# Kernel optimization log

Hardware: AMD Instinct MI355X
Metric: run time of the kernel (lower is better)

Reference implementation:

```python
import jax, jax.numpy as jnp
import numpy as np
from jax import lax

N, IN_C, H, W = 8, 256, 100, 100
MID_C = 256
RATIOS = (0.5, 1.0, 2.0)
SCALES = (8, 16, 32)
FEAT_STRIDE = 16
BASE_SIZE = 16.0
K = len(RATIOS) * len(SCALES)
NMS_THRESH = 0.7
PRE_NMS = 3000
POST_NMS = 300
MIN_SIZE = 16.0


def _anchor_base():
    py = px = BASE_SIZE / 2.0
    ab = np.zeros((K, 4), np.float32)
    i = 0
    for r in RATIOS:
        for s in SCALES:
            h = BASE_SIZE * s * np.sqrt(r)
            w = BASE_SIZE * s * np.sqrt(1.0 / r)
            ab[i] = [py - h / 2.0, px - w / 2.0, py + h / 2.0, px + w / 2.0]
            i += 1
    return ab


def _all_anchors():
    ab = _anchor_base()
    sy = np.arange(H, dtype=np.float32) * FEAT_STRIDE
    sx = np.arange(W, dtype=np.float32) * FEAT_STRIDE
    yy, xx = np.meshgrid(sy, sx, indexing="ij")
    shifts = np.stack([yy.ravel(), xx.ravel(), yy.ravel(), xx.ravel()], 1)  # [HW,4]
    anchors = (shifts[:, None, :] + ab[None, :, :]).reshape(-1, 4)  # (h,w,k) order -> [K*H*W,4]
    return jnp.asarray(anchors)


def _conv(x, w, b, pad):
    y = lax.conv_general_dilated(x, w, (1, 1), [(pad, pad), (pad, pad)],
                                 dimension_numbers=("NCHW", "OIHW", "NCHW"))
    return y + b[None, :, None, None]


def _decode(anchors, loc):  # reg2bbox: boxes in [y1,x1,y2,x2], loc = [dy,dx,dh,dw]
    ah = anchors[:, 2] - anchors[:, 0]
    aw = anchors[:, 3] - anchors[:, 1]
    ay = anchors[:, 0] + 0.5 * ah
    ax = anchors[:, 1] + 0.5 * aw
    dy, dx, dh, dw = loc[:, 0], loc[:, 1], loc[:, 2], loc[:, 3]
    cy = dy * ah + ay
    cx = dx * aw + ax
    h = jnp.exp(dh) * ah
    w = jnp.exp(dw) * aw
    return jnp.stack([cy - 0.5 * h, cx - 0.5 * w, cy + 0.5 * h, cx + 0.5 * w], 1)


def _greedy_nms(boxes, valid):  # boxes sorted by score desc; returns keep mask
    P = boxes.shape[0]
    y1, x1, y2, x2 = boxes[:, 0], boxes[:, 1], boxes[:, 2], boxes[:, 3]
    areas = (y2 - y1) * (x2 - x1)
    idx = jnp.arange(P)

    def body(i, keep):
        yy1 = jnp.maximum(y1[i], y1)
        xx1 = jnp.maximum(x1[i], x1)
        yy2 = jnp.minimum(y2[i], y2)
        xx2 = jnp.minimum(x2[i], x2)
        inter = jnp.maximum(yy2 - yy1, 0.0) * jnp.maximum(xx2 - xx1, 0.0)
        iou = inter / (areas[i] + areas - inter + 1e-9)
        suppress = (iou > NMS_THRESH) & (idx > i) & keep[i]
        return keep & (~suppress)

    return lax.fori_loop(0, P, body, valid)


def _propose(anchors, scores, loc, img_w, img_h):
    boxes = _decode(anchors, loc)
    y1 = jnp.clip(boxes[:, 0], 0.0, img_h)
    y2 = jnp.clip(boxes[:, 2], 0.0, img_h)
    x1 = jnp.clip(boxes[:, 1], 0.0, img_w)
    x2 = jnp.clip(boxes[:, 3], 0.0, img_w)
    boxes = jnp.stack([y1, x1, y2, x2], 1)
    big = ((y2 - y1) >= MIN_SIZE) & ((x2 - x1) >= MIN_SIZE)
    s = jnp.where(big, scores, -1.0)  # push filtered boxes to the bottom (softmax scores in [0,1])
    order = jnp.argsort(-s)[:PRE_NMS]
    b = boxes[order]
    v = big[order]
    keep = _greedy_nms(lax.stop_gradient(b), v)
    # kept boxes first, preserving score order (matches torchvision nms index order)
    rank = jnp.where(keep, jnp.arange(PRE_NMS), PRE_NMS + jnp.arange(PRE_NMS))
    sel = jnp.argsort(rank)[:POST_NMS]
    roi = b[sel] * keep[sel][:, None].astype(b.dtype)  # zero-pad suppressed slots
    return roi


def reference(x, w1, b1, wc, bc, wr, br, img_width, img_height):
    h = jax.nn.relu(_conv(x, w1, b1, 1))
    cls = _conv(h, wc, bc, 0)  # [N,2K,H,W]
    cls = jnp.transpose(cls, (0, 2, 3, 1)).reshape(N, -1, 2)  # [N,KHW,2]
    fg = jax.nn.softmax(cls, axis=-1)[:, :, 1]  # [N,KHW]
    cls_out = jnp.transpose(cls, (0, 2, 1))  # [N,2,KHW]
    reg = _conv(h, wr, br, 0)
    reg = jnp.transpose(reg, (0, 2, 3, 1)).reshape(N, -1, 4)  # [N,KHW,4]
    anchors = _all_anchors()
    rois = jax.vmap(_propose, in_axes=(None, 0, 0, None, None))(
        anchors, fg, reg, float(img_width), float(img_height))  # [N,POST_NMS,4]
    roi_inds = jnp.repeat(jnp.arange(N, dtype=jnp.float32), POST_NMS)
    return cls_out, reg, rois.reshape(-1, 4), roi_inds, anchors


def setup_inputs() -> dict:
    key = jax.random.key(0)
    ks = jax.random.split(key, 4)
    std = 0.01
    return {
        "x": jax.random.normal(ks[0], (N, IN_C, H, W), jnp.float32),
        "w1": std * jax.random.normal(ks[1], (MID_C, IN_C, 3, 3), jnp.float32),
        "b1": jnp.zeros((MID_C,), jnp.float32),
        "wc": std * jax.random.normal(ks[2], (2 * K, MID_C, 1, 1), jnp.float32),
        "bc": jnp.zeros((2 * K,), jnp.float32),
        "wr": std * jax.random.normal(ks[3], (4 * K, MID_C, 1, 1), jnp.float32),
        "br": jnp.zeros((4 * K,), jnp.float32),
        "img_width": 1600,
        "img_height": 1600,
    }
```

## Files before the change

### kernel.cpp

```cpp
#include <hip/hip_runtime.h>
#include <cstdint>
#include <math.h>

static constexpr int NB  = 8;
static constexpr int CC_ = 256;
static constexpr int HH  = 100, WW = 100, HW = 10000;
static constexpr int KA  = 9;
static constexpr int AN  = HW * KA;
static constexpr int PRE  = 3000;
static constexpr int POST = 300;
static constexpr int NW64 = 47;
static constexpr float NMS_T = 0.7f;

typedef _Float16 f16;
typedef _Float16 f16x8 __attribute__((ext_vector_type(8)));
typedef float f32x4 __attribute__((ext_vector_type(4)));

static constexpr size_t OUT_CLS  = 0;
static constexpr size_t OUT_REG  = 1440000;
static constexpr size_t OUT_ROIS = 4320000;
static constexpr size_t OUT_RIND = 4329600;
static constexpr size_t OUT_ANCH = 4332000;

static constexpr size_t WS_H     = 0;
static constexpr size_t WS_WT    = 81920000;
static constexpr size_t WS_W54   = WS_WT   + 2359296;
static constexpr size_t WS_BOXES = WS_W54  + 55296;
static constexpr size_t WS_KEYS  = WS_BOXES+ 11520000;
static constexpr size_t WS_SBOX  = WS_KEYS + 2880000;
static constexpr size_t WS_SVAL  = WS_SBOX + 384000;
static constexpr size_t WS_MASK  = WS_SVAL + 96000;

__device__ __constant__ float AHC[9] = {
  90.50966799187809f, 181.01933598375618f, 362.03867196751236f,
  128.f, 256.f, 512.f,
  181.01933598375618f, 362.03867196751236f, 724.0773439350247f };
__device__ __constant__ float AWC[9] = {
  181.01933598375618f, 362.03867196751236f, 724.0773439350247f,
  128.f, 256.f, 512.f,
  90.50966799187809f, 181.01933598375618f, 362.03867196751236f };

__global__ void k_prep_all(const float* __restrict__ w1, const float* __restrict__ wc,
                           const float* __restrict__ wr, f16* __restrict__ WH,
                           f16* __restrict__ WL, float* __restrict__ w54,
                           float* __restrict__ anch) {
  int t = blockIdx.x * 256 + threadIdx.x;
  if (t < 589824) {
    int cil = t & 7, co = (t >> 3) & 255, rr = t >> 11;
    int kq = rr & 3, kg = (rr >> 2) & 7, tap = rr >> 5;
    int ci = kg * 32 + kq * 8 + cil;
    float v = w1[((size_t)co * 256 + ci) * 9 + tap];
    f16 hi = (f16)v;
    float res = v - (float)hi;
    WH[t] = hi;
    WL[t] = (f16)(res * 2048.f);
  }
  if (t < 256 * 54) {
    int ci = t / 54, j = t % 54;
    w54[t] = (j < 18) ? wc[j * 256 + ci] : wr[(j - 18) * 256 + ci];
  }
  int u = t - 256 * 54;
  if (u >= 0 && u < AN) {
    int k = u % KA; int pp = u / KA; int y = pp / WW; int x = pp % WW;
    int ri = k / 3, si = k % 3;
    double scale = (double)(8 << si);
    double r = (ri == 0) ? 0.5 : ((ri == 1) ? 1.0 : 2.0);
    double hh = 16.0 * scale * sqrt(r);
    double ww = 16.0 * scale * sqrt(1.0 / r);
    double sy = y * 16.0, sx = x * 16.0;
    anch[(size_t)u * 4 + 0] = (float)(sy + 8.0 - hh * 0.5);
    anch[(size_t)u * 4 + 1] = (float)(sx + 8.0 - ww * 0.5);
    anch[(size_t)u * 4 + 2] = (float)(sy + 8.0 + hh * 0.5);
    anch[(size_t)u * 4 + 3] = (float)(sx + 8.0 + ww * 0.5);
  }
}

__global__ __launch_bounds__(256, 3) void k_conv3x3(const float* __restrict__ x,
    const f16* __restrict__ WH, const f16* __restrict__ WL,
    const float* __restrict__ b1, float* __restrict__ hout) {
  __shared__ __align__(16) f16 SX[2][2][4][180][8];
  const int tid = threadIdx.x;
  const int lane = tid & 63;
  const int w = tid >> 6;
  const int bid = blockIdx.x;
  const int p = ((bid >> 5) << 3) | (bid & 7);
  const int cotile = (bid >> 3) & 3;
  const int xt_yt = p % 91;
  const int n = p / 91;
  const int xt = xt_yt % 7, yt = xt_yt / 7;
  const int x0 = xt * 16, y0 = yt * 8;
  const int wy = (w & 1) * 4;
  const int wc = (w >> 1) * 32;
  const int xb = lane & 15, kh = lane >> 4;

  const int sp = tid;
  const bool s_on = sp < 180;
  const int s_r = sp / 18, s_c = sp % 18;
  const int gy = y0 - 1 + s_r, gx = x0 - 1 + s_c;
  const bool s_ok = s_on && gy >= 0 && gy < HH && gx >= 0 && gx < WW;
  const int s_goff = s_ok ? gy * WW + gx : 0;

  const float* xn = x + (size_t)n * CC_ * HW;

  f32x4 acc1[2][4], acc2[2][4];
  #pragma unroll
  for (int a = 0; a < 2; ++a)
    #pragma unroll
    for (int b = 0; b < 4; ++b) {
      acc1[a][b] = (f32x4){0.f, 0.f, 0.f, 0.f};
      acc2[a][b] = (f32x4){0.f, 0.f, 0.f, 0.f};
    }

  float xv[16];
  auto prefetch16 = [&](int kg2, int half) {
    if (s_ok) {
      const float* bp = xn + (size_t)(kg2 * 32 + half * 16) * HW + s_goff;
      #pragma unroll
      for (int j = 0; j < 16; ++j) xv[j] = bp[(size_t)j * HW];
    } else {
      #pragma unroll
      for (int j = 0; j < 16; ++j) xv[j] = 0.f;
    }
  };
  auto commit16 = [&](int nb, int half) {
    if (s_on) {
      #pragma unroll
      for (int q = 0; q < 2; ++q) {
        f16x8 H, L;
        #pragma unroll
        for (int j = 0; j < 8; ++j) {
          float v = xv[q * 8 + j];
          f16 hi = (f16)v;
          float res = v - (float)hi;
          H[j] = hi;
          L[j] = (f16)(res * 2048.f);
        }
        *(f16x8*)&SX[nb][0][half * 2 + q][sp][0] = H;
        *(f16x8*)&SX[nb][1][half * 2 + q][sp][0] = L;
      }
    }
  };

  const int cob = cotile * 64 + wc;
  auto loadA = [&](int kg2, int tap, f16x8* ah, f16x8* al) {
    const size_t wbase = ((((size_t)tap * 8 + kg2) * 4 + kh) * 256 + cob + xb) * 8;
    #pragma unroll
    for (int cf = 0; cf < 2; ++cf) {
      ah[cf] = *(const f16x8*)(WH + wbase + (size_t)cf * 128);
      al[cf] = *(const f16x8*)(WL + wbase + (size_t)cf * 128);
    }
  };

  prefetch16(0, 0); commit16(0, 0);
  prefetch16(0, 1); commit16(0, 1);
  __syncthreads();

  for (int kg = 0; kg < 8; ++kg) {
    const int buf = kg & 1;
    const bool more = (kg < 7);
    f16x8 ah[2][2], al[2][2];
    loadA(kg, 0, ah[0], al[0]);
    if (more) prefetch16(kg + 1, 0);
    __builtin_amdgcn_sched_barrier(0);
    #pragma unroll
    for (int kx = 0; kx < 3; ++kx) {
      f16x8 rh[6], rl[6];
      #pragma unroll
      for (int r = 0; r < 6; ++r) {
        const int pixf = (wy + r) * 18 + xb + kx;
        rh[r] = *(const f16x8*)&SX[buf][0][kh][pixf][0];
        rl[r] = *(const f16x8*)&SX[buf][1][kh][pixf][0];
      }
      #pragma unroll
      for (int ky = 0; ky < 3; ++ky) {
        const int s = kx * 3 + ky;
        const int cur = s & 1;
        if (s < 8) {
          const int s2 = s + 1;
          loadA(kg, (s2 % 3) * 3 + s2 / 3, ah[cur ^ 1], al[cur ^ 1]);
        }
        __builtin_amdgcn_sched_barrier(0);
        #pragma unroll
        for (int cf = 0; cf < 2; ++cf)
          #pragma unroll
          for (int nf = 0; nf < 4; ++nf) {
            acc1[cf][nf] = __builtin_amdgcn_mfma_f32_16x16x32_f16(ah[cur][cf], rh[nf + ky], acc1[cf][nf], 0, 0, 0);
            acc2[cf][nf] = __builtin_amdgcn_mfma_f32_16x16x32_f16(ah[cur][cf], rl[nf + ky], acc2[cf][nf], 0, 0, 0);
            acc2[cf][nf] = __builtin_amdgcn_mfma_f32_16x16x32_f16(al[cur][cf], rh[nf + ky], acc2[cf][nf], 0, 0, 0);
          }
      }
      if (kx == 1 && more) {
        commit16(buf ^ 1, 0);
        prefetch16(kg + 1, 1);
        __builtin_amdgcn_sched_barrier(0);
      }
    }
    if (more) commit16(buf ^ 1, 1);
    __syncthreads();
  }

  const int xg = x0 + xb;
  #pragma unroll
  for (int cf = 0; cf < 2; ++cf)
    #pragma unroll
    for (int r = 0; r < 4; ++r) {
      const int co = cob + cf * 16 + kh * 4 + r;
      const float bias = b1[co];
      const size_t obase = (size_t)(n * CC_ + co) * HH;
      #pragma unroll
      for (int nf = 0; nf < 4; ++nf) {
        const int yg = y0 + wy + nf;
        if (yg < HH && xg < WW) {
          float v = fmaf(acc2[cf][nf][r], 0.00048828125f, acc1[cf][nf][r]) + bias;
          hout[(obase + yg) * WW + xg] = fmaxf(v, 0.f);
        }
      }
    }
}

__global__ __launch_bounds__(256) void k_heads(const float* __restrict__ hin,
    const float* __restrict__ w54, const float* __restrict__ bc, const float* __restrict__ br,
    const int* __restrict__ imw, const int* __restrict__ imh,
    float* __restrict__ cls_out, float* __restrict__ reg_out,
    float* __restrict__ boxes, unsigned int* __restrict__ keys) {
  int gid = blockIdx.x * 256 + threadIdx.x;
  if (gid >= NB * HW) return;
  int n = gid / HW, p = gid % HW;
  float cacc[18], racc[36];
  #pragma unroll
  for (int j = 0; j < 18; ++j) cacc[j] = 0.f;
  #pragma unroll
  for (int j = 0; j < 36; ++j) racc[j] = 0.f;
  const float* hp = hin + (size_t)n * CC_ * HW + p;
  #pragma unroll 8
  for (int ci = 0; ci < CC_; ++ci) {
    float hv = hp[(size_t)ci * HW];
    const float* wrow = w54 + ci * 54;
    #pragma unroll
    for (int j = 0; j < 18; ++j) cacc[j] = fmaf(hv, wrow[j], cacc[j]);
    #pragma unroll
    for (int j = 0; j < 36; ++j) racc[j] = fmaf(hv, wrow[18 + j], racc[j]);
  }
  const float imgW = (float)imw[0], imgH = (float)imh[0];
  const int y = p / WW, xq = p % WW;
  #pragma unroll
  for (int k = 0; k < 9; ++k) {
    float c0 = cacc[2 * k] + bc[2 * k];
    float c1 = cacc[2 * k + 1] + bc[2 * k + 1];
    int a = p * 9 + k;
    cls_out[(size_t)n * 2 * AN + a]      = c0;
    cls_out[(size_t)n * 2 * AN + AN + a] = c1;
    float t0 = racc[4 * k]     + br[4 * k];
    float t1 = racc[4 * k + 1] + br[4 * k + 1];
    float t2 = racc[4 * k + 2] + br[4 * k + 2];
    float t3 = racc[4 * k + 3] + br[4 * k + 3];
    size_t ro = ((size_t)n * AN + a) * 4;
    reg_out[ro] = t0; reg_out[ro + 1] = t1; reg_out[ro + 2] = t2; reg_out[ro + 3] = t3;
    float hk = AHC[k], wk = AWC[k];
    float cy = fmaf(t0, hk, y  * 16.f + 8.f);
    float cx = fmaf(t1, wk, xq * 16.f + 8.f);
    float bh = expf(t2) * hk, bw = expf(t3) * wk;
    float y1 = cy - 0.5f * bh, x1 = cx - 0.5f * bw;
    float y2 = cy + 0.5f * bh, x2 = cx + 0.5f * bw;
    y1 = fminf(fmaxf(y1, 0.f), imgH); y2 = fminf(fmaxf(y2, 0.f), imgH);
    x1 = fminf(fmaxf(x1, 0.f), imgW); x2 = fminf(fmaxf(x2, 0.f), imgW);
    bool valid = (y2 - y1 >= 16.f) && (x2 - x1 >= 16.f);
    boxes[ro] = y1; boxes[ro + 1] = x1; boxes[ro + 2] = y2; boxes[ro + 3] = x2;
    float dc = c1 - c0;
    unsigned u = __float_as_uint(dc);
    u = (u & 0x80000000u) ? ~u : (u | 0x80000000u);
    keys[(size_t)n * AN + a] = valid ? u : 0u;
  }
}

__global__ __launch_bounds__(1024) void k_select(const unsigned* __restrict__ keys,
    const float* __restrict__ boxes, float* __restrict__ sbox, int* __restrict__ sval) {
  __shared__ unsigned hist[4][1024];
  __shared__ unsigned long long cand[4096];
  __shared__ int sB1, sA1, sB2, scnt;
  const int t = threadIdx.x;
  const int n = blockIdx.x;
  const unsigned* kp = keys + (size_t)n * AN;
  for (int i = t; i < 4096; i += 1024) ((unsigned*)hist)[i] = 0;
  __syncthreads();
  const int rep = (t >> 6) & 3;
  for (int i = t; i < AN; i += 1024) atomicAdd(&hist[rep][kp[i] >> 22], 1u);
  __syncthreads();
  unsigned myc = hist[0][t] + hist[1][t] + hist[2][t] + hist[3][t];
  __syncthreads();
  hist[0][t] = myc;
  __syncthreads();
  for (int off = 1; off < 1024; off <<= 1) {
    unsigned add = (t + off < 1024) ? hist[0][t + off] : 0;
    __syncthreads();
    hist[0][t] += add;
    __syncthreads();
  }
  unsigned incl = hist[0][t];
  unsigned above = incl - myc;
  if (above < (unsigned)PRE && incl >= (unsigned)PRE && myc > 0) { sB1 = t; sA1 = (int)above; }
  __syncthreads();
  const int B1 = sB1, A1 = sA1;
  __syncthreads();
  hist[0][t] = 0;
  __syncthreads();
  for (int i = t; i < AN; i += 1024) {
    unsigned k32 = kp[i];
    if ((int)(k32 >> 22) == B1) atomicAdd(&hist[0][(k32 >> 12) & 1023u], 1u);
  }
  __syncthreads();
  myc = hist[0][t];
  __syncthreads();
  for (int off = 1; off < 1024; off <<= 1) {
    unsigned add = (t + off < 1024) ? hist[0][t + off] : 0;
    __syncthreads();
    hist[0][t] += add;
    __syncthreads();
  }
  incl = hist[0][t]; above = incl - myc;
  const int target = PRE - A1;
  if ((int)above < target && (int)incl >= target && myc > 0) sB2 = t;
  if (t == 0) scnt = 0;
  __syncthreads();
  const int B2 = sB2;
  for (int i = t; i < AN; i += 1024) {
    unsigned k32 = kp[i];
    int b1 = (int)(k32 >> 22);
    bool sel = (b1 > B1) || (b1 == B1 && (int)((k32 >> 12) & 1023u) >= B2);
    if (sel) {
      int pos = atomicAdd(&scnt, 1);
      if (pos < 4096)
        cand[pos] = ((unsigned long long)k32 << 32) | (unsigned long long)(0xFFFFFFFFu - (unsigned)i);
    }
  }
  __syncthreads();
  int cnt = scnt; if (cnt > 4096) cnt = 4096;
  for (int i = cnt + t; i < 4096; i += 1024) cand[i] = 0ull;
  __syncthreads();
  for (int k = 2; k <= 4096; k <<= 1) {
    for (int j = k >> 1; j > 0; j >>= 1) {
      for (int i = t; i < 4096; i += 1024) {
        int ixj = i ^ j;
        if (ixj > i) {
          unsigned long long va = cand[i], vb = cand[ixj];
          bool desc = ((i & k) == 0);
          if (desc ? (va < vb) : (va > vb)) { cand[i] = vb; cand[ixj] = va; }
        }
      }
      __syncthreads();
    }
  }
  for (int i = t; i < PRE; i += 1024) {
    unsigned long long kv = cand[i];
    unsigned idx = 0xFFFFFFFFu - (unsigned)(kv & 0xFFFFFFFFull);
    float4 bb = *(const float4*)(boxes + ((size_t)n * AN + idx) * 4);
    *(float4*)(sbox + ((size_t)n * PRE + i) * 4) = bb;
    sval[n * PRE + i] = ((kv >> 32) != 0ull) ? 1 : 0;
  }
}

__global__ __launch_bounds__(256) void k_mask(const float* __restrict__ sbox,
    unsigned long long* __restrict__ mask) {
  __shared__ float4 jb[64];
  const int t = threadIdx.x;
  const int lane = t & 63, wv = t >> 6;
  const int jt = blockIdx.x, n = blockIdx.z;
  const int it = blockIdx.y * 4 + wv;
  const int j0 = jt * 64;
  if (t < 64) {
    int jg = j0 + t;
    float4 v = make_float4(0.f, 0.f, 0.f, 0.f);
    if (jg < PRE) v = *(const float4*)(sbox + ((size_t)n * PRE + jg) * 4);
    jb[t] = v;
  }
  __syncthreads();
  const int i = it * 64 + lane;
  if (it >= NW64 || i >= PRE) return;
  float4 bi = *(const float4*)(sbox + ((size_t)n * PRE + i) * 4);
  float areaI = (bi.z - bi.x) * (bi.w - bi.y);
  unsigned long long bits = 0ull;
  #pragma unroll 4
  for (int jj = 0; jj < 64; ++jj) {
    int j = j0 + jj;
    float4 bj = jb[jj];
    float yy1 = fmaxf(bi.x, bj.x), xx1 = fmaxf(bi.y, bj.y);
    float yy2 = fminf(bi.z, bj.z), xx2 = fminf(bi.w, bj.w);
    float inter = fmaxf(yy2 - yy1, 0.f) * fmaxf(xx2 - xx1, 0.f);
    float areaJ = (bj.z - bj.x) * (bj.w - bj.y);
    float iou = inter / (areaI + areaJ - inter + 1e-9f);
    if (iou > NMS_T && j > i && j < PRE) bits |= (1ull << jj);
  }
  mask[((size_t)n * 3008 + i) * NW64 + jt] = bits;
}

__global__ __launch_bounds__(256) void k_nms_final(const unsigned long long* __restrict__ mask,
    const int* __restrict__ sval, const float* __restrict__ sbox,
    float* __restrict__ rois, float* __restrict__ rind) {
  __shared__ unsigned long long kws[NW64];
  __shared__ int pref[NW64 + 1];
  const int t = threadIdx.x, n = blockIdx.x;
  if (t < 64) {
    unsigned long long keep = 0ull;
    for (int w = 0; w < NW64; ++w) {
      int i = w * 64 + t;
      int v = (i < PRE) ? sval[n * PRE + i] : 0;
      unsigned long long m = __ballot(v != 0);
      if (t == w) keep = m;
    }
    const unsigned long long* mrow = mask + (size_t)n * 3008 * NW64;
    unsigned long long buf[16];
    #pragma unroll
    for (int r = 0; r < 16; ++r)
      buf[r] = (t < NW64) ? mrow[(size_t)r * NW64 + t] : 0ull;
    for (int base = 0; base < PRE; base += 16) {
      #pragma unroll
      for (int r = 0; r < 16; ++r) {
        int i = base + r;
        if (i < PRE) {
          unsigned long long kb = __shfl(keep, i >> 6);
          if ((kb >> (i & 63)) & 1ull) keep &= ~buf[r];
        }
        int nx = i + 16;
        buf[r] = (nx < PRE && t < NW64) ? mrow[(size_t)nx * NW64 + t] : 0ull;
      }
    }
    if (t < NW64) kws[t] = keep;
  }
  __syncthreads();
  if (t == 0) {
    int s = 0;
    for (int w = 0; w < NW64; ++w) { pref[w] = s; s += __popcll(kws[w]); }
    pref[NW64] = s;
  }
  for (int e = t; e < POST * 4; e += 256) rois[(size_t)n * POST * 4 + e] = 0.f;
  for (int e = t; e < POST; e += 256) rind[(size_t)n * POST + e] = (float)n;
  __syncthreads();
  for (int i = t; i < PRE; i += 256) {
    int wd = i >> 6, b = i & 63;
    unsigned long long wv = kws[wd];
    if ((wv >> b) & 1ull) {
      int rank = pref[wd] + __popcll(wv & ((1ull << b) - 1ull));
      if (rank < POST) {
        float4 bb = *(const float4*)(sbox + ((size_t)n * PRE + i) * 4);
        *(float4*)(rois + ((size_t)n * POST + rank) * 4) = bb;
      }
    }
  }
}

extern "C" void kernel_launch(void* const* d_in, const int* in_sizes, int n_in,
                              void* d_out, int out_size, void* d_ws, size_t ws_size,
                              hipStream_t stream) {
  const float* x  = (const float*)d_in[0];
  const float* w1 = (const float*)d_in[1];
  const float* b1 = (const float*)d_in[2];
  const float* wc = (const float*)d_in[3];
  const float* bc = (const float*)d_in[4];
  const float* wr = (const float*)d_in[5];
  const float* br = (const float*)d_in[6];
  const int* imw  = (const int*)d_in[7];
  const int* imh  = (const int*)d_in[8];
  float* out = (float*)d_out;
  char* ws = (char*)d_ws;
  float* hbuf = (float*)(ws + WS_H);
  f16* WH     = (f16*)(ws + WS_WT);
  f16* WL     = (f16*)(ws + WS_WT + 1179648);
  float* w54  = (float*)(ws + WS_W54);
  float* boxes = (float*)(ws + WS_BOXES);
  unsigned* keys = (unsigned*)(ws + WS_KEYS);
  float* sbox = (float*)(ws + WS_SBOX);
  int* sval   = (int*)(ws + WS_SVAL);
  unsigned long long* mask  = (unsigned long long*)(ws + WS_MASK);

  k_prep_all<<<2304, 256, 0, stream>>>(w1, wc, wr, WH, WL, w54, out + OUT_ANCH);
  k_conv3x3<<<2912, 256, 0, stream>>>(x, WH, WL, b1, hbuf);
  k_heads<<<313, 256, 0, stream>>>(hbuf, w54, bc, br, imw, imh,
                                   out + OUT_CLS, out + OUT_REG, boxes, keys);
  k_select<<<NB, 1024, 0, stream>>>(keys, boxes, sbox, sval);
  k_mask<<<dim3(NW64, 12, NB), 256, 0, stream>>>(sbox, mask);
  k_nms_final<<<NB, 256, 0, stream>>>(mask, sval, sbox, out + OUT_ROIS, out + OUT_RIND);
}
```

Before: 1.108 ms.

## Split top-k selection into multi-block histogram, threshold, compact and sort kernels

The single 8-block selection kernel is replaced by a pipeline of kernels. Histogram and compaction passes now run on 32 blocks per image, merging counts through global atomics. Small threshold kernels compute the radix cut points, and a final kernel sorts the compacted candidates. The global histogram, metadata and candidate buffers are zeroed in the prep kernel. This spreads the repeated 90k-key scans across many CUs, at the cost of more launches and global atomic traffic.

```diff
diff --git a/kernel.cpp b/kernel.cpp
--- a/kernel.cpp
+++ b/kernel.cpp
@@ -30,6 +30,11 @@
 static constexpr size_t WS_SBOX  = WS_KEYS + 2880000;
 static constexpr size_t WS_SVAL  = WS_SBOX + 384000;
 static constexpr size_t WS_MASK  = WS_SVAL + 96000;
+static constexpr size_t SEL_H1   = 0;
+static constexpr size_t SEL_H2   = 32768;
+static constexpr size_t SEL_META = 65536;
+static constexpr size_t SEL_CAND = 65792;
+static constexpr int    SEL_ZERO_U32 = 81984;
 
 __device__ __constant__ float AHC[9] = {
   90.50966799187809f, 181.01933598375618f, 362.03867196751236f,
@@ -43,8 +48,9 @@
 __global__ void k_prep_all(const float* __restrict__ w1, const float* __restrict__ wc,
                            const float* __restrict__ wr, f16* __restrict__ WH,
                            f16* __restrict__ WL, float* __restrict__ w54,
-                           float* __restrict__ anch) {
+                           float* __restrict__ anch, unsigned* __restrict__ selz) {
   int t = blockIdx.x * 256 + threadIdx.x;
+  if (t < SEL_ZERO_U32) selz[t] = 0u;
   if (t < 589824) {
     int cil = t & 7, co = (t >> 3) & 255, rr = t >> 11;
     int kq = rr & 3, kg = (rr >> 2) & 7, tap = rr >> 5;
@@ -273,69 +279,114 @@
   }
 }
 
-__global__ __launch_bounds__(1024) void k_select(const unsigned* __restrict__ keys,
-    const float* __restrict__ boxes, float* __restrict__ sbox, int* __restrict__ sval) {
-  __shared__ unsigned hist[4][1024];
-  __shared__ unsigned long long cand[4096];
-  __shared__ int sB1, sA1, sB2, scnt;
-  const int t = threadIdx.x;
-  const int n = blockIdx.x;
+__global__ __launch_bounds__(256) void k_sel_hist1(const unsigned* __restrict__ keys,
+    unsigned* __restrict__ hist1) {
+  __shared__ unsigned h[4][1024];
+  const int t = threadIdx.x, n = blockIdx.y;
+  for (int i = t; i < 4096; i += 256) ((unsigned*)h)[i] = 0;
+  __syncthreads();
   const unsigned* kp = keys + (size_t)n * AN;
-  for (int i = t; i < 4096; i += 1024) ((unsigned*)hist)[i] = 0;
-  __syncthreads();
-  const int rep = (t >> 6) & 3;
-  for (int i = t; i < AN; i += 1024) atomicAdd(&hist[rep][kp[i] >> 22], 1u);
-  __syncthreads();
-  unsigned myc = hist[0][t] + hist[1][t] + hist[2][t] + hist[3][t];
-  __syncthreads();
-  hist[0][t] = myc;
+  const int wv = t >> 6;
+  for (int i = blockIdx.x * 256 + t; i < AN; i += 32 * 256)
+    atomicAdd(&h[wv][kp[i] >> 22], 1u);
+  __syncthreads();
+  for (int b = t; b < 1024; b += 256) {
+    unsigned s = h[0][b] + h[1][b] + h[2][b] + h[3][b];
+    if (s) atomicAdd(&hist1[n * 1024 + b], s);
+  }
+}
+
+__global__ __launch_bounds__(1024) void k_sel_thresh1(const unsigned* __restrict__ hist1,
+    int* __restrict__ meta) {
+  __shared__ unsigned sc[1024];
+  __shared__ int sB1, sA1;
+  const int t = threadIdx.x, n = blockIdx.x;
+  unsigned myc = hist1[n * 1024 + t];
+  sc[t] = myc;
   __syncthreads();
   for (int off = 1; off < 1024; off <<= 1) {
-    unsigned add = (t + off < 1024) ? hist[0][t + off] : 0;
+    unsigned add = (t + off < 1024) ? sc[t + off] : 0;
     __syncthreads();
-    hist[0][t] += add;
+    sc[t] += add;
     __syncthreads();
   }
-  unsigned incl = hist[0][t];
+  unsigned incl = sc[t];
   unsigned above = incl - myc;
   if (above < (unsigned)PRE && incl >= (unsigned)PRE && myc > 0) { sB1 = t; sA1 = (int)above; }
   __syncthreads();
-  const int B1 = sB1, A1 = sA1;
-  __syncthreads();
-  hist[0][t] = 0;
-  __syncthreads();
-  for (int i = t; i < AN; i += 1024) {
+  if (t == 0) { meta[n * 4 + 0] = sB1; meta[n * 4 + 1] = sA1; }
+}
+
+__global__ __launch_bounds__(256) void k_sel_hist2(const unsigned* __restrict__ keys,
+    const int* __restrict__ meta, unsigned* __restrict__ hist2) {
+  __shared__ unsigned h[4][1024];
+  __shared__ int sB1;
+  const int t = threadIdx.x, n = blockIdx.y;
+  if (t == 0) sB1 = meta[n * 4 + 0];
+  for (int i = t; i < 4096; i += 256) ((unsigned*)h)[i] = 0;
+  __syncthreads();
+  const int B1 = sB1;
+  const unsigned* kp = keys + (size_t)n * AN;
+  const int wv = t >> 6;
+  for (int i = blockIdx.x * 256 + t; i < AN; i += 32 * 256) {
     unsigned k32 = kp[i];
-    if ((int)(k32 >> 22) == B1) atomicAdd(&hist[0][(k32 >> 12) & 1023u], 1u);
-  }
-  __syncthreads();
-  myc = hist[0][t];
+    if ((int)(k32 >> 22) == B1) atomicAdd(&h[wv][(k32 >> 12) & 1023u], 1u);
+  }
+  __syncthreads();
+  for (int b = t; b < 1024; b += 256) {
+    unsigned s = h[0][b] + h[1][b] + h[2][b] + h[3][b];
+    if (s) atomicAdd(&hist2[n * 1024 + b], s);
+  }
+}
+
+__global__ __launch_bounds__(1024) void k_sel_thresh2(const unsigned* __restrict__ hist2,
+    int* __restrict__ meta) {
+  __shared__ unsigned sc[1024];
+  __shared__ int sB2;
+  const int t = threadIdx.x, n = blockIdx.x;
+  unsigned myc = hist2[n * 1024 + t];
+  sc[t] = myc;
   __syncthreads();
   for (int off = 1; off < 1024; off <<= 1) {
-    unsigned add = (t + off < 1024) ? hist[0][t + off] : 0;
+    unsigned add = (t + off < 1024) ? sc[t + off] : 0;
     __syncthreads();
-    hist[0][t] += add;
+    sc[t] += add;
     __syncthreads();
   }
-  incl = hist[0][t]; above = incl - myc;
-  const int target = PRE - A1;
+  unsigned incl = sc[t];
+  unsigned above = incl - myc;
+  const int target = PRE - meta[n * 4 + 1];
   if ((int)above < target && (int)incl >= target && myc > 0) sB2 = t;
-  if (t == 0) scnt = 0;
-  __syncthreads();
-  const int B2 = sB2;
-  for (int i = t; i < AN; i += 1024) {
+  __syncthreads();
+  if (t == 0) meta[n * 4 + 2] = sB2;
+}
+
+__global__ __launch_bounds__(256) void k_sel_compact(const unsigned* __restrict__ keys,
+    int* __restrict__ meta, unsigned long long* __restrict__ cand) {
+  __shared__ int sB1, sB2;
+  const int t = threadIdx.x, n = blockIdx.y;
+  if (t == 0) { sB1 = meta[n * 4 + 0]; sB2 = meta[n * 4 + 2]; }
+  __syncthreads();
+  const int B1 = sB1, B2 = sB2;
+  const unsigned* kp = keys + (size_t)n * AN;
+  for (int i = blockIdx.x * 256 + t; i < AN; i += 32 * 256) {
     unsigned k32 = kp[i];
     int b1 = (int)(k32 >> 22);
     bool sel = (b1 > B1) || (b1 == B1 && (int)((k32 >> 12) & 1023u) >= B2);
     if (sel) {
-      int pos = atomicAdd(&scnt, 1);
+      int pos = atomicAdd(&meta[n * 4 + 3], 1);
       if (pos < 4096)
-        cand[pos] = ((unsigned long long)k32 << 32) | (unsigned long long)(0xFFFFFFFFu - (unsigned)i);
-    }
-  }
-  __syncthreads();
-  int cnt = scnt; if (cnt > 4096) cnt = 4096;
-  for (int i = cnt + t; i < 4096; i += 1024) cand[i] = 0ull;
+        cand[(size_t)n * 4096 + pos] =
+          ((unsigned long long)k32 << 32) | (unsigned long long)(0xFFFFFFFFu - (unsigned)i);
+    }
+  }
+}
+
+__global__ __launch_bounds__(1024) void k_sel_sort(const unsigned long long* __restrict__ candg,
+    const float* __restrict__ boxes, float* __restrict__ sbox, int* __restrict__ sval) {
+  __shared__ unsigned long long cand[4096];
+  const int t = threadIdx.x, n = blockIdx.x;
+  for (int i = t; i < 4096; i += 1024) cand[i] = candg[(size_t)n * 4096 + i];
   __syncthreads();
   for (int k = 2; k <= 4096; k <<= 1) {
     for (int j = k >> 1; j > 0; j >>= 1) {
@@ -471,12 +522,21 @@
   float* sbox = (float*)(ws + WS_SBOX);
   int* sval   = (int*)(ws + WS_SVAL);
   unsigned long long* mask  = (unsigned long long*)(ws + WS_MASK);
-
-  k_prep_all<<<2304, 256, 0, stream>>>(w1, wc, wr, WH, WL, w54, out + OUT_ANCH);
+  unsigned* sel_h1 = (unsigned*)(ws + WS_MASK + SEL_H1);
+  unsigned* sel_h2 = (unsigned*)(ws + WS_MASK + SEL_H2);
+  int* sel_meta    = (int*)(ws + WS_MASK + SEL_META);
+  unsigned long long* sel_cand = (unsigned long long*)(ws + WS_MASK + SEL_CAND);
+
+  k_prep_all<<<2304, 256, 0, stream>>>(w1, wc, wr, WH, WL, w54, out + OUT_ANCH, sel_h1);
   k_conv3x3<<<2912, 256, 0, stream>>>(x, WH, WL, b1, hbuf);
   k_heads<<<313, 256, 0, stream>>>(hbuf, w54, bc, br, imw, imh,
                                    out + OUT_CLS, out + OUT_REG, boxes, keys);
-  k_select<<<NB, 1024, 0, stream>>>(keys, boxes, sbox, sval);
+  k_sel_hist1<<<dim3(32, NB), 256, 0, stream>>>(keys, sel_h1);
+  k_sel_thresh1<<<NB, 1024, 0, stream>>>(sel_h1, sel_meta);
+  k_sel_hist2<<<dim3(32, NB), 256, 0, stream>>>(keys, sel_meta, sel_h2);
+  k_sel_thresh2<<<NB, 1024, 0, stream>>>(sel_h2, sel_meta);
+  k_sel_compact<<<dim3(32, NB), 256, 0, stream>>>(keys, sel_meta, sel_cand);
+  k_sel_sort<<<NB, 1024, 0, stream>>>(sel_cand, boxes, sbox, sval);
   k_mask<<<dim3(NW64, 12, NB), 256, 0, stream>>>(sbox, mask);
   k_nms_final<<<NB, 256, 0, stream>>>(mask, sval, sbox, out + OUT_ROIS, out + OUT_RIND);
 }
```

After: 1.123 ms. Within noise of the previous version (+1.4%).
